# Optimization experiments

Measured on AMD Instinct MI355X. Metric: run time of the kernel, lower is better.

The kernel has to match this reference:

```python
import jax, jax.numpy as jnp
import numpy as np
import math

BASE_RES = 16
MAX_RES = 2048
LEVELS = 16
FEAT_DIM = 2
LOG_B = math.log(MAX_RES / BASE_RES) / (LEVELS - 1)  # per-level log scale


def setup_inputs() -> dict:
    key = jax.random.key(0)
    k1, k2 = jax.random.split(key)
    B = 1048576
    positions = jax.random.uniform(k1, (B, 3), dtype=jnp.float32)
    total = MAX_RES * MAX_RES * 3 * FEAT_DIM
    # torch.nn.init.uniform_ -> U[0,1)
    plane_table = jax.random.uniform(k2, (total,), dtype=jnp.float32)
    return {"positions": positions, "plane_table": plane_table}


def _encode(positions, plane_table):
    B = positions.shape[0]
    dtype = positions.dtype
    # planes: (xy, yz, zx) -> [B, 3 planes, 2 coords]
    x, y, z = positions[:, 0], positions[:, 1], positions[:, 2]
    xyz6 = jnp.stack([x, y, y, z, z, x], axis=1).reshape(B, 3, 2)
    planes = plane_table.reshape(3, MAX_RES * MAX_RES, FEAT_DIM)
    plane_ids = jnp.arange(3)  # [3]
    outs = []
    for level in range(LEVELS):
        scale = BASE_RES * math.exp(level * LOG_B) - 1.0
        res = int(math.ceil(scale)) + 1  # grid_resolution
        pos = xyz6 * (res - 1) + 0.5            # [B,3,2]
        pg = jnp.floor(pos)
        frac = pos - pg                          # fractional part
        pg = pg.astype(jnp.int32)
        local = jnp.zeros((B, 3, FEAT_DIM), dtype)
        for idx in range(4):  # 4 bilinear corners
            w = jnp.ones((B, 3), dtype)
            coords = []
            for d in range(2):
                if idx & (1 << d):
                    coords.append(pg[..., d] + 1)
                    w = w * frac[..., d]
                else:
                    coords.append(pg[..., d])
                    w = w * (1.0 - frac[..., d])
            c = jnp.stack(coords, axis=-1).astype(dtype)  # [B,3,2]
            # remap corner from level grid to the max_res storage grid (truncating cast)
            c_ori = (c / res * (MAX_RES - 1)).astype(jnp.int32)
            index = c_ori[..., 0] + c_ori[..., 1] * MAX_RES  # [B,3] flat plane index
            feats = planes[plane_ids[None, :], index]        # [B,3,FEAT_DIM] gather
            local = local + w[..., None] * feats
        # cross-plane product
        outs.append(local[:, 0] * local[:, 1] * local[:, 2])  # [B,FEAT_DIM]
    out = jnp.stack(outs, axis=2)  # [B, FEAT_DIM, LEVELS]; sn = j*LEVELS + level
    return out.reshape(B, FEAT_DIM * LEVELS)


def reference(positions, plane_table):
    return _encode(positions, plane_table)
```

## Files before the change

kernel.cpp:

```cpp
#include <hip/hip_runtime.h>
#include <math.h>

#define LEVELS 16
#define MAX_RES 2048
#define NCELL_BITS 5
#define NCELLS (1 << (3 * NCELL_BITS))
#define LC_LO 9
#define LC_HI 12

typedef float nfloat4 __attribute__((ext_vector_type(4)));
typedef float nfloat2 __attribute__((ext_vector_type(2)));

struct ResParams {
  int res[LEVELS];
  int coff[LEVELS];
  int S[LEVELS];
};


__device__ __forceinline__ unsigned int morton5(int cx, int cy, int cz) {
  unsigned int k = 0;
  #pragma unroll
  for (int b = 0; b < NCELL_BITS; ++b)
    k |= (((cx >> b) & 1) << (3 * b)) | (((cy >> b) & 1) << (3 * b + 1)) |
         (((cz >> b) & 1) << (3 * b + 2));
  return k;
}

__device__ __forceinline__ unsigned int cell_of(float x, float y, float z) {
  int cx = min(31, max(0, (int)(x * 32.0f)));
  int cy = min(31, max(0, (int)(y * 32.0f)));
  int cz = min(31, max(0, (int)(z * 32.0f)));
  return morton5(cx, cy, cz);
}

__global__ __launch_bounds__(256) void keys_hist(const float* __restrict__ pos,
                                                 unsigned int* __restrict__ hist, int B) {
  int i = blockIdx.x * 256 + threadIdx.x;
  if (i >= B) return;
  atomicAdd(&hist[cell_of(pos[i*3], pos[i*3+1], pos[i*3+2])], 1u);
}

__global__ __launch_bounds__(1024) void scan_kernel(const unsigned int* __restrict__ hist,
                                                    unsigned int* __restrict__ offs) {
  __shared__ unsigned int part[1024];
  const int SEG = NCELLS / 1024;
  int t = threadIdx.x;
  int base = t * SEG;
  unsigned int s = 0;
  #pragma unroll
  for (int j = 0; j < SEG; ++j) s += hist[base + j];
  part[t] = s;
  __syncthreads();
  for (int off = 1; off < 1024; off <<= 1) {
    unsigned int v = (t >= off) ? part[t - off] : 0u;
    __syncthreads();
    part[t] += v;
    __syncthreads();
  }
  unsigned int run = part[t] - s;
  #pragma unroll
  for (int j = 0; j < SEG; ++j) {
    unsigned int c = hist[base + j];
    offs[base + j] = run;
    run += c;
  }
}

__global__ __launch_bounds__(256) void scatter_kernel(const float* __restrict__ pos,
                                                      unsigned int* __restrict__ offs,
                                                      nfloat4* __restrict__ sorted, int B) {
  int i = blockIdx.x * 256 + threadIdx.x;
  if (i >= B) return;
  float x = pos[i*3], y = pos[i*3+1], z = pos[i*3+2];
  unsigned int slot = atomicAdd(&offs[cell_of(x, y, z)], 1u);
  nfloat4 v = {x, y, z, __int_as_float(i)};
  sorted[slot] = v;
}

__global__ __launch_bounds__(256) void build_compact(const float* __restrict__ table,
                                                     float2* __restrict__ compact,
                                                     ResParams P) {
  __shared__ nfloat2 rowbuf[MAX_RES];
  int l = LC_LO + blockIdx.y;
  int res = P.res[l];
  int W = res + 1;
  int bx = blockIdx.x;
  if (bx >= 3 * W) return;
  int p = bx / W;
  int v = bx - p * W;
  const float fres = (float)res;

  int cv = (int)(__fmul_rn(__fdiv_rn((float)v, fres), 2047.0f));
  const float* src = table + (size_t)p * (MAX_RES * MAX_RES * 2) + (size_t)(cv << 11) * 2;

  const nfloat4* src4 = reinterpret_cast<const nfloat4*>(src);
  #pragma unroll
  for (int j = (int)threadIdx.x; j < MAX_RES / 2; j += 256) {
    nfloat4 r = src4[j];
    rowbuf[j * 2]     = nfloat2{r.x, r.y};
    rowbuf[j * 2 + 1] = nfloat2{r.z, r.w};
  }
  __syncthreads();

  float2* dst = compact + (P.coff[l] + p * P.S[l] + v * W);
  for (int u = (int)threadIdx.x; u < W; u += 256) {
    int cu = (int)(__fmul_rn(__fdiv_rn((float)u, fres), 2047.0f));
    nfloat2 e = rowbuf[cu];
    dst[u] = make_float2(e.x, e.y);
  }
}


template <bool USE_COMPACT>
__global__ __launch_bounds__(256) void triplane_main(
    const nfloat4* __restrict__ sorted,
    const float* __restrict__ table,
    const float2* __restrict__ compact,
    float* __restrict__ out,
    ResParams P, int B, int nwg)
{
  int wg = blockIdx.x;
  int q = nwg >> 3, r = nwg & 7;
  int xcd = wg & 7, idx = wg >> 3;
  int swz = (xcd < r) ? xcd * (q + 1) + idx : r * (q + 1) + (xcd - r) * q + idx;
  int t = swz * 256 + (int)threadIdx.x;
  if (t >= B) return;

  nfloat4 s = sorted[t];
  float x = s.x, y = s.y, z = s.z;
  int orig = __float_as_int(s.w);

  float uarr[3] = {x, y, z};
  float varr[3] = {y, z, x};

  float o0[LEVELS], o1[LEVELS];

  #pragma unroll
  for (int l = 0; l < LEVELS; ++l) {
    const int   res   = P.res[l];
    const float resm1 = (float)(res - 1);
    const float fres  = (float)res;
    const bool  cpath = USE_COMPACT && (l >= LC_LO && l <= LC_HI);

    float prod0 = 1.0f, prod1 = 1.0f;

    #pragma unroll
    for (int p = 0; p < 3; ++p) {
      float pu = __fadd_rn(__fmul_rn(uarr[p], resm1), 0.5f);
      float pv = __fadd_rn(__fmul_rn(varr[p], resm1), 0.5f);
      float gu = floorf(pu), gv = floorf(pv);
      float fu = __fsub_rn(pu, gu);
      float fv = __fsub_rn(pv, gv);

      float f00x, f00y, f10x, f10y, f01x, f01y, f11x, f11y;

      if (cpath) {
        int iu = (int)gu, iv = (int)gv;
        int W = res + 1;
        const float2* lv = compact + (P.coff[l] + p * P.S[l]);
        int i0 = iv * W + iu;
        const nfloat4 r0 = *reinterpret_cast<const nfloat4*>(lv + i0);
        const nfloat4 r1 = *reinterpret_cast<const nfloat4*>(lv + i0 + W);
        f00x = r0.x; f00y = r0.y; f10x = r0.z; f10y = r0.w;
        f01x = r1.x; f01y = r1.y; f11x = r1.z; f11y = r1.w;
      } else {
        float gu1 = __fadd_rn(gu, 1.0f);
        float gv1 = __fadd_rn(gv, 1.0f);
        int cou0 = (int)(__fmul_rn(__fdiv_rn(gu,  fres), 2047.0f));
        int cou1 = (int)(__fmul_rn(__fdiv_rn(gu1, fres), 2047.0f));
        int cov0 = (int)(__fmul_rn(__fdiv_rn(gv,  fres), 2047.0f));
        int cov1 = (int)(__fmul_rn(__fdiv_rn(gv1, fres), 2047.0f));

        const float* plane = table + (size_t)p * (MAX_RES * MAX_RES * 2);

        if (l == 15) {
          const nfloat4 r0 = *reinterpret_cast<const nfloat4*>(plane + (size_t)(cou0 + (cov0 << 11)) * 2);
          const nfloat4 r1 = *reinterpret_cast<const nfloat4*>(plane + (size_t)(cou0 + (cov1 << 11)) * 2);
          const bool adj = (cou1 != cou0);
          f00x = r0.x; f00y = r0.y;
          f10x = adj ? r0.z : r0.x;  f10y = adj ? r0.w : r0.y;
          f01x = r1.x; f01y = r1.y;
          f11x = adj ? r1.z : r1.x;  f11y = adj ? r1.w : r1.y;
        } else {
          const float2 f00 = *reinterpret_cast<const float2*>(plane + (size_t)(cou0 + (cov0 << 11)) * 2);
          const float2 f10 = *reinterpret_cast<const float2*>(plane + (size_t)(cou1 + (cov0 << 11)) * 2);
          const float2 f01 = *reinterpret_cast<const float2*>(plane + (size_t)(cou0 + (cov1 << 11)) * 2);
          const float2 f11 = *reinterpret_cast<const float2*>(plane + (size_t)(cou1 + (cov1 << 11)) * 2);
          f00x = f00.x; f00y = f00.y; f10x = f10.x; f10y = f10.y;
          f01x = f01.x; f01y = f01.y; f11x = f11.x; f11y = f11.y;
        }
      }

      float w00 = (1.0f - fu) * (1.0f - fv);
      float w10 = fu * (1.0f - fv);
      float w01 = (1.0f - fu) * fv;
      float w11 = fu * fv;

      float a0 = 0.0f, a1 = 0.0f;
      a0 += w00 * f00x;  a1 += w00 * f00y;
      a0 += w10 * f10x;  a1 += w10 * f10y;
      a0 += w01 * f01x;  a1 += w01 * f01y;
      a0 += w11 * f11x;  a1 += w11 * f11y;

      prod0 *= a0;
      prod1 *= a1;
    }

    o0[l] = prod0;
    o1[l] = prod1;
  }

  nfloat4* base = reinterpret_cast<nfloat4*>(out + (size_t)orig * 32);
  #pragma unroll
  for (int k = 0; k < 4; ++k) {
    nfloat4 v0 = {o0[k*4+0], o0[k*4+1], o0[k*4+2], o0[k*4+3]};
    nfloat4 v1 = {o1[k*4+0], o1[k*4+1], o1[k*4+2], o1[k*4+3]};
    base[k] = v0;
    base[4 + k] = v1;
  }
}

extern "C" void kernel_launch(void* const* d_in, const int* in_sizes, int n_in,
                              void* d_out, int out_size, void* d_ws, size_t ws_size,
                              hipStream_t stream) {
  const float* positions = (const float*)d_in[0];
  const float* table     = (const float*)d_in[1];
  float* out             = (float*)d_out;
  int B = in_sizes[0] / 3;

  ResParams P;
  const double LOG_B = log(2048.0 / 16.0) / (double)(LEVELS - 1);
  int runoff = 0, Wmax = 0;
  for (int l = 0; l < LEVELS; ++l) {
    double scale = 16.0 * exp((double)l * LOG_B) - 1.0;
    P.res[l] = (int)ceil(scale) + 1;
    P.coff[l] = 0; P.S[l] = 0;
  }
  for (int l = LC_LO; l <= LC_HI; ++l) {
    int W = P.res[l] + 1;
    P.S[l] = W * W;
    P.coff[l] = runoff;
    runoff += 3 * P.S[l];
    if (W > Wmax) Wmax = W;
  }

  int nwg = (B + 255) / 256;

  size_t off_hist    = 0;
  size_t off_offs    = off_hist + (size_t)NCELLS * 4;
  size_t off_sorted  = off_offs + (size_t)NCELLS * 4;
  size_t off_compact = off_sorted + (size_t)B * 16;
  size_t need_sort   = off_compact;
  size_t need_all    = off_compact + (size_t)runoff * 8;

  if (ws_size < need_sort) return;

  unsigned int* hist = (unsigned int*)((char*)d_ws + off_hist);
  unsigned int* offs = (unsigned int*)((char*)d_ws + off_offs);
  nfloat4*      srt  = (nfloat4*)((char*)d_ws + off_sorted);
  float2*       cmp  = (float2*)((char*)d_ws + off_compact);

  const bool use_compact = (ws_size >= need_all);

  if (use_compact) {
    int ny = LC_HI - LC_LO + 1;
    hipLaunchKernelGGL(build_compact, dim3(3 * Wmax, ny), dim3(256), 0, stream, table, cmp, P);
  }

  hipMemsetAsync(hist, 0, (size_t)NCELLS * 4, stream);
  hipLaunchKernelGGL(keys_hist, dim3(nwg), dim3(256), 0, stream, positions, hist, B);
  hipLaunchKernelGGL(scan_kernel, dim3(1), dim3(1024), 0, stream, hist, offs);
  hipLaunchKernelGGL(scatter_kernel, dim3(nwg), dim3(256), 0, stream, positions, offs, srt, B);

  if (use_compact) {
    hipLaunchKernelGGL((triplane_main<true>), dim3(nwg), dim3(256), 0, stream,
                       srt, table, cmp, out, P, B, nwg);
  } else {
    hipLaunchKernelGGL((triplane_main<false>), dim3(nwg), dim3(256), 0, stream,
                       srt, table, cmp, out, P, B, nwg);
  }
}
```

Measured before the change: 452.5 us.

## Fuse compact-table build with histogram and split scan into multi-block passes

Merges the compact-table build kernel and the position histogram kernel into one launch, using a flattened block range per level so that no padded blocks exit early. Replaces the single-block 1024-thread scan with a per-256-cell block scan plus a 128-entry root scan, and the scatter adds the root offset. This aims to cut launch count, remove idle blocks, and parallelize the serial scan, at the cost of one extra small kernel and a per-block branch in the fused kernel.

Result: no change. 451.6 us (-0.2%).

```diff
diff --git a/kernel.cpp b/kernel.cpp
--- a/kernel.cpp
+++ b/kernel.cpp
@@ -7,6 +7,7 @@
 #define NCELLS (1 << (3 * NCELL_BITS))
 #define LC_LO 9
 #define LC_HI 12
+#define NLC (LC_HI - LC_LO + 1)
 
 typedef float nfloat4 __attribute__((ext_vector_type(4)));
 typedef float nfloat2 __attribute__((ext_vector_type(2)));
@@ -15,6 +16,7 @@
   int res[LEVELS];
   int coff[LEVELS];
   int S[LEVELS];
+  int bstart[NLC + 1];
 };
 
 
@@ -34,81 +36,99 @@
   return morton5(cx, cy, cz);
 }
 
-__global__ __launch_bounds__(256) void keys_hist(const float* __restrict__ pos,
-                                                 unsigned int* __restrict__ hist, int B) {
-  int i = blockIdx.x * 256 + threadIdx.x;
-  if (i >= B) return;
-  atomicAdd(&hist[cell_of(pos[i*3], pos[i*3+1], pos[i*3+2])], 1u);
-}
-
-__global__ __launch_bounds__(1024) void scan_kernel(const unsigned int* __restrict__ hist,
-                                                    unsigned int* __restrict__ offs) {
-  __shared__ unsigned int part[1024];
-  const int SEG = NCELLS / 1024;
-  int t = threadIdx.x;
-  int base = t * SEG;
-  unsigned int s = 0;
-  #pragma unroll
-  for (int j = 0; j < SEG; ++j) s += hist[base + j];
-  part[t] = s;
+__global__ __launch_bounds__(256) void build_and_hist(
+    const float* __restrict__ table, float2* __restrict__ compact,
+    const float* __restrict__ pos, unsigned int* __restrict__ hist,
+    ResParams P, int B, int nbuild)
+{
+  __shared__ nfloat2 rowbuf[MAX_RES];
+  int b = blockIdx.x;
+
+  if (b < nbuild) {
+    int li = 0;
+    #pragma unroll
+    for (int k = 1; k < NLC; ++k) if (b >= P.bstart[k]) li = k;
+    int l = LC_LO + li;
+    int res = P.res[l];
+    int W = res + 1;
+    int rem = b - P.bstart[li];
+    int p = rem / W;
+    int v = rem - p * W;
+    const float fres = (float)res;
+
+    int cv = (int)(__fmul_rn(__fdiv_rn((float)v, fres), 2047.0f));
+    const float* src = table + (size_t)p * (MAX_RES * MAX_RES * 2) + (size_t)(cv << 11) * 2;
+
+    const nfloat4* src4 = reinterpret_cast<const nfloat4*>(src);
+    #pragma unroll
+    for (int j = (int)threadIdx.x; j < MAX_RES / 2; j += 256) {
+      nfloat4 r = src4[j];
+      rowbuf[j * 2]     = nfloat2{r.x, r.y};
+      rowbuf[j * 2 + 1] = nfloat2{r.z, r.w};
+    }
+    __syncthreads();
+
+    float2* dst = compact + (P.coff[l] + p * P.S[l] + v * W);
+    for (int u = (int)threadIdx.x; u < W; u += 256) {
+      int cu = (int)(__fmul_rn(__fdiv_rn((float)u, fres), 2047.0f));
+      nfloat2 e = rowbuf[cu];
+      dst[u] = make_float2(e.x, e.y);
+    }
+  } else {
+    int i = (b - nbuild) * 256 + (int)threadIdx.x;
+    if (i < B)
+      atomicAdd(&hist[cell_of(pos[i*3], pos[i*3+1], pos[i*3+2])], 1u);
+  }
+}
+
+__global__ __launch_bounds__(256) void scan_partial(const unsigned int* __restrict__ hist,
+                                                    unsigned int* __restrict__ offs,
+                                                    unsigned int* __restrict__ partials) {
+  __shared__ unsigned int sh[256];
+  int tid = (int)threadIdx.x;
+  int c = blockIdx.x * 256 + tid;
+  unsigned int v = hist[c];
+  sh[tid] = v;
   __syncthreads();
-  for (int off = 1; off < 1024; off <<= 1) {
-    unsigned int v = (t >= off) ? part[t - off] : 0u;
-    __syncthreads();
-    part[t] += v;
-    __syncthreads();
-  }
-  unsigned int run = part[t] - s;
-  #pragma unroll
-  for (int j = 0; j < SEG; ++j) {
-    unsigned int c = hist[base + j];
-    offs[base + j] = run;
-    run += c;
-  }
+  #pragma unroll
+  for (int off = 1; off < 256; off <<= 1) {
+    unsigned int u = (tid >= off) ? sh[tid - off] : 0u;
+    __syncthreads();
+    sh[tid] += u;
+    __syncthreads();
+  }
+  offs[c] = sh[tid] - v;
+  if (tid == 255) partials[blockIdx.x] = sh[255];
+}
+
+__global__ __launch_bounds__(128) void scan_roots(unsigned int* __restrict__ partials,
+                                                  unsigned int* __restrict__ roots) {
+  __shared__ unsigned int sh[128];
+  int tid = (int)threadIdx.x;
+  unsigned int v = partials[tid];
+  sh[tid] = v;
+  __syncthreads();
+  #pragma unroll
+  for (int off = 1; off < 128; off <<= 1) {
+    unsigned int u = (tid >= off) ? sh[tid - off] : 0u;
+    __syncthreads();
+    sh[tid] += u;
+    __syncthreads();
+  }
+  roots[tid] = sh[tid] - v;
 }
 
 __global__ __launch_bounds__(256) void scatter_kernel(const float* __restrict__ pos,
                                                       unsigned int* __restrict__ offs,
+                                                      const unsigned int* __restrict__ roots,
                                                       nfloat4* __restrict__ sorted, int B) {
-  int i = blockIdx.x * 256 + threadIdx.x;
+  int i = blockIdx.x * 256 + (int)threadIdx.x;
   if (i >= B) return;
   float x = pos[i*3], y = pos[i*3+1], z = pos[i*3+2];
-  unsigned int slot = atomicAdd(&offs[cell_of(x, y, z)], 1u);
+  unsigned int k = cell_of(x, y, z);
+  unsigned int slot = roots[k >> 8] + atomicAdd(&offs[k], 1u);
   nfloat4 v = {x, y, z, __int_as_float(i)};
   sorted[slot] = v;
-}
-
-__global__ __launch_bounds__(256) void build_compact(const float* __restrict__ table,
-                                                     float2* __restrict__ compact,
-                                                     ResParams P) {
-  __shared__ nfloat2 rowbuf[MAX_RES];
-  int l = LC_LO + blockIdx.y;
-  int res = P.res[l];
-  int W = res + 1;
-  int bx = blockIdx.x;
-  if (bx >= 3 * W) return;
-  int p = bx / W;
-  int v = bx - p * W;
-  const float fres = (float)res;
-
-  int cv = (int)(__fmul_rn(__fdiv_rn((float)v, fres), 2047.0f));
-  const float* src = table + (size_t)p * (MAX_RES * MAX_RES * 2) + (size_t)(cv << 11) * 2;
-
-  const nfloat4* src4 = reinterpret_cast<const nfloat4*>(src);
-  #pragma unroll
-  for (int j = (int)threadIdx.x; j < MAX_RES / 2; j += 256) {
-    nfloat4 r = src4[j];
-    rowbuf[j * 2]     = nfloat2{r.x, r.y};
-    rowbuf[j * 2 + 1] = nfloat2{r.z, r.w};
-  }
-  __syncthreads();
-
-  float2* dst = compact + (P.coff[l] + p * P.S[l] + v * W);
-  for (int u = (int)threadIdx.x; u < W; u += 256) {
-    int cu = (int)(__fmul_rn(__fdiv_rn((float)u, fres), 2047.0f));
-    nfloat2 e = rowbuf[cu];
-    dst[u] = make_float2(e.x, e.y);
-  }
 }
 
 
@@ -231,47 +251,54 @@
 
   ResParams P;
   const double LOG_B = log(2048.0 / 16.0) / (double)(LEVELS - 1);
-  int runoff = 0, Wmax = 0;
+  int runoff = 0;
   for (int l = 0; l < LEVELS; ++l) {
     double scale = 16.0 * exp((double)l * LOG_B) - 1.0;
     P.res[l] = (int)ceil(scale) + 1;
     P.coff[l] = 0; P.S[l] = 0;
   }
-  for (int l = LC_LO; l <= LC_HI; ++l) {
+  int nbuild = 0;
+  for (int li = 0; li < NLC; ++li) {
+    int l = LC_LO + li;
     int W = P.res[l] + 1;
     P.S[l] = W * W;
     P.coff[l] = runoff;
     runoff += 3 * P.S[l];
-    if (W > Wmax) Wmax = W;
-  }
+    P.bstart[li] = nbuild;
+    nbuild += 3 * W;
+  }
+  P.bstart[NLC] = nbuild;
 
   int nwg = (B + 255) / 256;
 
   size_t off_hist    = 0;
   size_t off_offs    = off_hist + (size_t)NCELLS * 4;
-  size_t off_sorted  = off_offs + (size_t)NCELLS * 4;
+  size_t off_part    = off_offs + (size_t)NCELLS * 4;
+  size_t off_roots   = off_part + 128 * 4;
+  size_t off_sorted  = ((off_roots + 128 * 4) + 255) & ~(size_t)255;
   size_t off_compact = off_sorted + (size_t)B * 16;
   size_t need_sort   = off_compact;
   size_t need_all    = off_compact + (size_t)runoff * 8;
 
   if (ws_size < need_sort) return;
 
-  unsigned int* hist = (unsigned int*)((char*)d_ws + off_hist);
-  unsigned int* offs = (unsigned int*)((char*)d_ws + off_offs);
-  nfloat4*      srt  = (nfloat4*)((char*)d_ws + off_sorted);
-  float2*       cmp  = (float2*)((char*)d_ws + off_compact);
+  unsigned int* hist  = (unsigned int*)((char*)d_ws + off_hist);
+  unsigned int* offs  = (unsigned int*)((char*)d_ws + off_offs);
+  unsigned int* part  = (unsigned int*)((char*)d_ws + off_part);
+  unsigned int* roots = (unsigned int*)((char*)d_ws + off_roots);
+  nfloat4*      srt   = (nfloat4*)((char*)d_ws + off_sorted);
+  float2*       cmp   = (float2*)((char*)d_ws + off_compact);
 
   const bool use_compact = (ws_size >= need_all);
-
-  if (use_compact) {
-    int ny = LC_HI - LC_LO + 1;
-    hipLaunchKernelGGL(build_compact, dim3(3 * Wmax, ny), dim3(256), 0, stream, table, cmp, P);
-  }
+  const int nb = use_compact ? nbuild : 0;
 
   hipMemsetAsync(hist, 0, (size_t)NCELLS * 4, stream);
-  hipLaunchKernelGGL(keys_hist, dim3(nwg), dim3(256), 0, stream, positions, hist, B);
-  hipLaunchKernelGGL(scan_kernel, dim3(1), dim3(1024), 0, stream, hist, offs);
-  hipLaunchKernelGGL(scatter_kernel, dim3(nwg), dim3(256), 0, stream, positions, offs, srt, B);
+  hipLaunchKernelGGL(build_and_hist, dim3(nb + nwg), dim3(256), 0, stream,
+                     table, cmp, positions, hist, P, B, nb);
+  hipLaunchKernelGGL(scan_partial, dim3(NCELLS / 256), dim3(256), 0, stream, hist, offs, part);
+  hipLaunchKernelGGL(scan_roots, dim3(1), dim3(128), 0, stream, part, roots);
+  hipLaunchKernelGGL(scatter_kernel, dim3(nwg), dim3(256), 0, stream,
+                     positions, offs, roots, srt, B);
 
   if (use_compact) {
     hipLaunchKernelGGL((triplane_main<true>), dim3(nwg), dim3(256), 0, stream,
```
